# Optimization experiments

Hardware: AMD Instinct MI355X
Metric: run time of the kernel (lower is better)

## Reference

```python
import jax, jax.numpy as jnp
import numpy as np

B, P, N, E = 32, 1024, 1024, 128
HQ = 128  # head_num * qkv_dim == embedding_dim
SQRT_E = 11.313708498984761
LOGIT_CLIP = 10.0


def setup_inputs() -> dict:
    key = jax.random.key(0)
    ks = jax.random.split(key, 16)
    s = 1.0 / np.sqrt(E)
    return {
        "encoded_nodes": jax.random.normal(ks[0], (B, N, E), jnp.float32),
        "encoded_q1": jax.random.normal(ks[1], (B, P, E), jnp.float32),
        "encoded_q2": jax.random.normal(ks[2], (B, P, E), jnp.float32),
        "encoded_last_node": jax.random.normal(ks[3], (B, P, E), jnp.float32),
        "load": jax.random.uniform(ks[4], (B, P), jnp.float32),
        "left": jax.random.uniform(ks[5], (B, P), jnp.float32),
        "cur_dist": jax.random.uniform(ks[6], (B, P, N), jnp.float32),
        "log_scale": jnp.ones((), jnp.float32),
        "ninf_mask": jnp.zeros((B, P, N), jnp.float32),
        "Wq1": jax.random.normal(ks[7], (E, HQ), jnp.float32) * s,
        "Wq2": jax.random.normal(ks[8], (E, HQ), jnp.float32) * s,
        "Wq_last": jax.random.normal(ks[9], (E + 2, HQ), jnp.float32) * s,
        "Wk": jax.random.normal(ks[10], (E, HQ), jnp.float32) * s,
        "Wv": jax.random.normal(ks[11], (E, HQ), jnp.float32) * s,
        "AFT_dist_alpha": jnp.ones((1,), jnp.float32),
        "probs_dist_alpha": jnp.ones((1,), jnp.float32),
    }


def reference(encoded_nodes, encoded_q1, encoded_q2, encoded_last_node, load, left,
              cur_dist, log_scale, ninf_mask, Wq1, Wq2, Wq_last, Wk, Wv,
              AFT_dist_alpha, probs_dist_alpha):
    # set_kv / set_q1 / set_q2
    k = encoded_nodes @ Wk                      # [B,N,HQ]
    v = encoded_nodes @ Wv                      # [B,N,HQ]
    single_head_key = jnp.swapaxes(encoded_nodes, 1, 2)  # [B,E,N]
    q1 = encoded_q1 @ Wq1                       # [B,P,HQ]
    q2 = encoded_q2 @ Wq2

    input_cat = jnp.concatenate([encoded_last_node, load[:, :, None], left[:, :, None]], axis=2)
    q_last = input_cat @ Wq_last                # [B,P,HQ]
    q = q1 + q2 + q_last

    cur_dist_out = -cur_dist                    # [B,P,N]
    sigmoid_q = jax.nn.sigmoid(q)
    bias_scale = log_scale * AFT_dist_alpha[0] * cur_dist_out + ninf_mask
    e_bias = jnp.exp(bias_scale)                # [B,P,N]
    ek = jnp.exp(k)                             # [B,N,HQ]
    num = jnp.nan_to_num(jnp.einsum('bpn,bnd->bpd', e_bias, ek * v))
    den = jnp.nan_to_num(jnp.einsum('bpn,bnd->bpd', e_bias, ek)) + 1e-20
    AFT_out = sigmoid_q * (num / den)           # [B,P,HQ]

    score = jnp.einsum('bpd,bdn->bpn', AFT_out, single_head_key)
    score_scaled = score / SQRT_E + log_scale * probs_dist_alpha[0] * cur_dist_out
    score_clipped = LOGIT_CLIP * jnp.tanh(score_scaled)
    probs = jax.nn.softmax(score_clipped + ninf_mask, axis=2)
    return probs
```

## Files before the change

kernel.cpp:

```cpp
#include <hip/hip_runtime.h>
#include <math.h>

#define Bb 32
#define Pp 1024
#define Nn 1024

typedef unsigned short u16;
typedef __bf16 bf16x8 __attribute__((ext_vector_type(8)));
typedef float f32x4 __attribute__((ext_vector_type(4)));
typedef u16 us8 __attribute__((ext_vector_type(8)));
typedef u16 us4 __attribute__((ext_vector_type(4)));

#define MFMA __builtin_amdgcn_mfma_f32_16x16x32_bf16

static constexpr float INV_SQRT_E = 0.08838834764831845f;

__device__ __forceinline__ bf16x8 asbf(us8 v) { return __builtin_bit_cast(bf16x8, v); }

__device__ __forceinline__ void bsplit(float x, u16& h, u16& l) {
  unsigned u = __float_as_uint(x);
  unsigned r = u + 0x7FFF + ((u >> 16) & 1);
  h = (u16)(r >> 16);
  float hf = __uint_as_float((unsigned)h << 16);
  float lof = x - hf;
  unsigned u2 = __float_as_uint(lof);
  unsigned r2 = u2 + 0x7FFF + ((u2 >> 16) & 1);
  l = (u16)(r2 >> 16);
}

__device__ __forceinline__ void tsplit(float x, u16& h, u16& l) {
  unsigned u = __float_as_uint(x);
  h = (u16)(u >> 16);
  float lof = x - __uint_as_float(u & 0xFFFF0000u);
  l = (u16)(__float_as_uint(lof) >> 16);
}

__device__ __forceinline__ float fast_tanh(float x) {
  float ax = fabsf(x);
  float t = __expf(-2.0f * ax);
  float r = (1.0f - t) / (1.0f + t);
  return copysignf(r, x);
}

__global__ __launch_bounds__(256) void prep_weights(
    const float* __restrict__ Wq1, const float* __restrict__ Wq2,
    const float* __restrict__ Wql, const float* __restrict__ Wk,
    const float* __restrict__ Wv, u16* __restrict__ wcat_hi, u16* __restrict__ wcat_lo,
    u16* __restrict__ wkv_hi, u16* __restrict__ wkv_lo) {
  int t = threadIdx.x;
  if (blockIdx.x == 0) {
    for (int i = t; i < 128 * 384; i += 256) {
      int c = i / 384, k = i % 384;
      float v = (k < 128) ? Wq1[k * 128 + c]
                          : (k < 256) ? Wq2[(k - 128) * 128 + c] : Wql[(k - 256) * 128 + c];
      u16 h, l;
      bsplit(v, h, l);
      wcat_hi[i] = h;
      wcat_lo[i] = l;
    }
  } else {
    for (int i = t; i < 256 * 128; i += 256) {
      int c = i >> 7, k = i & 127;
      float v = (c < 128) ? Wk[k * 128 + c] : Wv[k * 128 + (c - 128)];
      u16 h, l;
      bsplit(v, h, l);
      wkv_hi[i] = h;
      wkv_lo[i] = l;
    }
  }
}

__global__ __launch_bounds__(256, 1) void kv_prep(
    const float* __restrict__ nodes, const u16* __restrict__ wkv_hi,
    const u16* __restrict__ wkv_lo, u16* __restrict__ ekkP_hi, u16* __restrict__ ekkP_lo,
    u16* __restrict__ nodesP_hi, u16* __restrict__ nodesP_lo) {
  __shared__ u16 a_hi[32 * 136], a_lo[32 * 136];
  __shared__ float kvbuf[32 * 264];
  const int t = threadIdx.x;
  const int xcd = blockIdx.x & 7, jj = blockIdx.x >> 3;
  const int b = xcd * 4 + (jj >> 5);
  const int n0 = (jj & 31) * 32;
  for (int i = t; i < 4096; i += 256) {
    int n = i >> 7, d = i & 127;
    float v = nodes[((long)(b * 1024 + n0 + n)) * 128 + d];
    u16 h, l;
    bsplit(v, h, l);
    a_hi[n * 136 + d] = h;
    a_lo[n * 136 + d] = l;
  }
  __syncthreads();
  const int lane = t & 63, w = t >> 6;
  const int lr = lane & 15, lg = lane >> 4;
  f32x4 acc0[2][4] = {}, acc1[2][4] = {};
#pragma unroll
  for (int ks = 0; ks < 4; ++ks) {
    us8 ah[2], al[2];
#pragma unroll
    for (int mt = 0; mt < 2; ++mt) {
      int ro = (lr + 16 * mt) * 136 + ks * 32 + lg * 8;
      ah[mt] = *(const us8*)&a_hi[ro];
      al[mt] = *(const us8*)&a_lo[ro];
    }
    us8 bh[4], bl[4];
#pragma unroll
    for (int cc = 0; cc < 4; ++cc) {
      long off = (long)((w * 4 + cc) * 16 + lr) * 128 + ks * 32 + lg * 8;
      bh[cc] = *(const us8*)&wkv_hi[off];
      bl[cc] = *(const us8*)&wkv_lo[off];
    }
#pragma unroll
    for (int mt = 0; mt < 2; ++mt)
#pragma unroll
      for (int cc = 0; cc < 4; ++cc) {
        acc0[mt][cc] = MFMA(asbf(ah[mt]), asbf(bh[cc]), acc0[mt][cc], 0, 0, 0);
        acc1[mt][cc] = MFMA(asbf(al[mt]), asbf(bh[cc]), acc1[mt][cc], 0, 0, 0);
        acc1[mt][cc] = MFMA(asbf(ah[mt]), asbf(bl[cc]), acc1[mt][cc], 0, 0, 0);
      }
  }
#pragma unroll
  for (int mt = 0; mt < 2; ++mt)
#pragma unroll
    for (int cc = 0; cc < 4; ++cc) {
      int c = (w * 4 + cc) * 16 + lr;
#pragma unroll
      for (int r = 0; r < 4; ++r)
        kvbuf[(lg * 4 + r + 16 * mt) * 264 + c] = acc0[mt][cc][r] + acc1[mt][cc][r];
    }
  __syncthreads();
#pragma unroll
  for (int jo = 0; jo < 4; ++jo) {
    int c = jo * 64 + (t & 63);
    int i4 = t >> 6;
    int kcol = (c < 128) ? c : (c - 128);
    us8 h8, l8;
#pragma unroll
    for (int jq = 0; jq < 8; ++jq) {
      int n = i4 * 8 + jq;
      float kv = kvbuf[n * 264 + kcol];
      float ek = __expf(kv);
      float val = (c < 128) ? ek * kvbuf[n * 264 + c + 128] : ek;
      u16 h, l;
      bsplit(val, h, l);
      h8[jq] = h;
      l8[jq] = l;
    }
    long o = (((long)b * 128 + (n0 >> 3) + i4) * 256 + c) * 8;
    *(us8*)&ekkP_hi[o] = h8;
    *(us8*)&ekkP_lo[o] = l8;
  }
  {
    int pl = t >> 7, r = t & 127;
    int dgrp = r >> 3, nb = r & 7;
    const u16* src = pl ? a_lo : a_hi;
    u16* dst = pl ? nodesP_lo : nodesP_hi;
#pragma unroll
    for (int i = 0; i < 4; ++i) {
      int n = nb + 8 * i;
      us8 v = *(const us8*)&src[n * 136 + dgrp * 8];
      *(us8*)&dst[(((long)(b * 16 + dgrp)) * 1024 + n0 + n) * 8] = v;
    }
  }
}

__global__ __launch_bounds__(256) void qsig_prep(
    const float* __restrict__ q1m, const float* __restrict__ q2m,
    const float* __restrict__ lnm, const float* __restrict__ loadv,
    const float* __restrict__ leftv, const float* __restrict__ Wql,
    const u16* __restrict__ wcat_hi, const u16* __restrict__ wcat_lo,
    float* __restrict__ qsig) {
  const int t = threadIdx.x;
  const int lane = t & 63, w = t >> 6;
  const int lr = lane & 15, lg = lane >> 4;
  const long p0 = (long)blockIdx.x * 16;
  const long arow = p0 + lr;
  f32x4 qacc[2] = {};
#pragma unroll 2
  for (int s = 0; s < 12; ++s) {
    const float* __restrict__ src = (s < 4) ? q1m : (s < 8) ? q2m : lnm;
    long ao = arow * 128 + (s & 3) * 32 + lg * 8;
    float4 a0 = *(const float4*)&src[ao];
    float4 a1 = *(const float4*)&src[ao + 4];
    float av[8] = {a0.x, a0.y, a0.z, a0.w, a1.x, a1.y, a1.z, a1.w};
    us8 ah, al;
#pragma unroll
    for (int jq = 0; jq < 8; ++jq) {
      u16 hh, ll;
      tsplit(av[jq], hh, ll);
      ah[jq] = hh;
      al[jq] = ll;
    }
#pragma unroll
    for (int cf = 0; cf < 2; ++cf) {
      int c = w * 32 + cf * 16 + lr;
      us8 bh = *(const us8*)&wcat_hi[c * 384 + s * 32 + lg * 8];
      us8 bl = *(const us8*)&wcat_lo[c * 384 + s * 32 + lg * 8];
      qacc[cf] = MFMA(asbf(ah), asbf(bh), qacc[cf], 0, 0, 0);
      qacc[cf] = MFMA(asbf(al), asbf(bh), qacc[cf], 0, 0, 0);
      qacc[cf] = MFMA(asbf(ah), asbf(bl), qacc[cf], 0, 0, 0);
    }
  }
#pragma unroll
  for (int cf = 0; cf < 2; ++cf) {
    int c = w * 32 + cf * 16 + lr;
    float wl1 = Wql[128 * 128 + c], wl2 = Wql[129 * 128 + c];
#pragma unroll
    for (int r = 0; r < 4; ++r) {
      int row = lg * 4 + r;
      float qv = qacc[cf][r] + loadv[p0 + row] * wl1 + leftv[p0 + row] * wl2;
      qsig[(p0 + row) * 128 + c] = 1.0f / (1.0f + __expf(-qv));
    }
  }
}

__global__ __launch_bounds__(256, 2) void ndaft_gemm(
    const float* __restrict__ cdist, const float* __restrict__ ninf,
    const u16* __restrict__ ekkP_hi, const u16* __restrict__ ekkP_lo,
    const float* __restrict__ qsig, u16* __restrict__ aftP_hi,
    u16* __restrict__ aftP_lo, u16* __restrict__ bias16,
    const float* __restrict__ logs, const float* __restrict__ aal,
    const float* __restrict__ pal) {
  __shared__ u16 lds[20480];
  const int t = threadIdx.x;
  const int lane = t & 63, w = t >> 6;
  const int lr = lane & 15, lg = lane >> 4;
  const int wr = w >> 1, wc = w & 1;
  const int xcd = blockIdx.x & 7, g = blockIdx.x >> 3;
  const int b = xcd * 4 + (g & 3);
  const int pt = g >> 2;
  const long bp = (long)b * Pp + pt * 64;
  const float c1 = logs[0] * aal[0];
  const float c2 = logs[0] * pal[0];

  const int srow = t >> 2, soct = t & 3;
  const long arow = bp + srow;
  const long tbase = (arow >> 4) * 32768;
  const int pr = srow & 15, ptile = srow >> 4;

  float4 d0, d1, f0, f1;
  us8 bst[8];
  auto load_regs = [&](int s) {
    long ao = arow * 1024 + s * 32 + soct * 8;
    d0 = *(const float4*)&cdist[ao];
    d1 = *(const float4*)&cdist[ao + 4];
    f0 = *(const float4*)&ninf[ao];
    f1 = *(const float4*)&ninf[ao + 4];
#pragma unroll
    for (int i = 0; i < 8; ++i) {
      int u = i * 256 + t;
      int oct = u >> 9, pl = (u >> 8) & 1, c = u & 255;
      const u16* bP = pl ? ekkP_lo : ekkP_hi;
      bst[i] = *(const us8*)&bP[(((long)b * 128 + s * 4 + oct) * 256 + c) * 8];
    }
  };

  us8 ebh, ebl;
  auto compute_eb = [&](int s) {
    float dv[8] = {d0.x, d0.y, d0.z, d0.w, d1.x, d1.y, d1.z, d1.w};
    float nv[8] = {f0.x, f0.y, f0.z, f0.w, f1.x, f1.y, f1.z, f1.w};
    us8 q8;
#pragma unroll
    for (int jq = 0; jq < 8; ++jq) {
      float e = __expf(fmaf(-c1, dv[jq], nv[jq]));
      u16 h, l;
      tsplit(e, h, l);
      ebh[jq] = h;
      ebl[jq] = l;
      float x = fminf(fmaxf(c2 * dv[jq], 0.f), 15.999f);
      q8[jq] = (nv[jq] < -1e5f) ? (u16)0xFFFF : (u16)(x * 4096.f + 0.5f);
    }
    *(us8*)&bias16[tbase + ((s * 4 + soct) * 16 + pr) * 8] = q8;
  };

  auto write_lds = [&]() {
    *(us8*)&lds[((ptile * 2 + 0) * 4 + soct) * 128 + pr * 8] = ebh;
    *(us8*)&lds[((ptile * 2 + 1) * 4 + soct) * 128 + pr * 8] = ebl;
#pragma unroll
    for (int i = 0; i < 8; ++i) {
      int u = i * 256 + t;
      int oct = u >> 9, pl = (u >> 8) & 1, c = u & 255;
      *(us8*)&lds[4096 + ((oct * 2 + pl) * 256 + c) * 8] = bst[i];
    }
  };

  f32x4 acc[2][8] = {};
  load_regs(0);
  for (int s = 0; s < 32; ++s) {
    compute_eb(s);
    __syncthreads();
    write_lds();
    __syncthreads();
    if (s < 31) load_regs(s + 1);
    us8 ah[2], al[2];
#pragma unroll
    for (int mt = 0; mt < 2; ++mt) {
      int ptl = wr * 2 + mt;
      ah[mt] = *(const us8*)&lds[((ptl * 2 + 0) * 4 + lg) * 128 + lr * 8];
      al[mt] = *(const us8*)&lds[((ptl * 2 + 1) * 4 + lg) * 128 + lr * 8];
    }
#pragma unroll
    for (int ct = 0; ct < 8; ++ct) {
      int c = (ct < 4) ? (wc * 64 + ct * 16 + lr) : (128 + wc * 64 + (ct - 4) * 16 + lr);
      us8 bh = *(const us8*)&lds[4096 + ((lg * 2 + 0) * 256 + c) * 8];
      us8 bl = *(const us8*)&lds[4096 + ((lg * 2 + 1) * 256 + c) * 8];
#pragma unroll
      for (int mt = 0; mt < 2; ++mt) {
        acc[mt][ct] = MFMA(asbf(ah[mt]), asbf(bh), acc[mt][ct], 0, 0, 0);
        acc[mt][ct] = MFMA(asbf(al[mt]), asbf(bh), acc[mt][ct], 0, 0, 0);
        acc[mt][ct] = MFMA(asbf(ah[mt]), asbf(bl), acc[mt][ct], 0, 0, 0);
      }
    }
  }
#pragma unroll
  for (int mt = 0; mt < 2; ++mt)
#pragma unroll
    for (int ct = 0; ct < 4; ++ct) {
      int cn = wc * 64 + ct * 16 + lr;
      int nc = cn >> 3, jq = cn & 7;
#pragma unroll
      for (int r = 0; r < 4; ++r) {
        long gr = bp + wr * 32 + mt * 16 + lg * 4 + r;
        float sig = qsig[gr * 128 + cn];
        float aftv = sig * (acc[mt][ct][r] / (acc[mt][ct + 4][r] + 1e-20f));
        u16 h, l;
        bsplit(aftv, h, l);
        long idx = (gr >> 4) * 2048 + (nc * 16 + (gr & 15)) * 8 + jq;
        aftP_hi[idx] = h;
        aftP_lo[idx] = l;
      }
    }
}

__global__ __launch_bounds__(512, 4) void score_softmax(
    const u16* bias16, const u16* __restrict__ aftP_hi, const u16* __restrict__ aftP_lo,
    const u16* __restrict__ nodesP_hi, const u16* __restrict__ nodesP_lo,
    float* out) {
  __shared__ float sbuf[32 * 264];
  __shared__ float psum[32 * 4];
  __shared__ float invb[32];
  const int t = threadIdx.x;
  const int lane = t & 63, w = t >> 6;
  const int lr = lane & 15, lg = lane >> 4;
  const int rg = w & 1, cg = w >> 1;
  const int xcd = blockIdx.x & 7, j = blockIdx.x >> 3;
  const int b = xcd * 4 + (j >> 5);
  const int p0 = (j & 31) * 32;
  const long bp = (long)b * Pp + p0;
  const int tileb = b * 64 + (p0 >> 4);

  f32x4 sacc[16] = {};
#pragma unroll
  for (int ks = 0; ks < 4; ++ks) {
    long aoff = (long)(tileb + rg) * 2048 + ((long)((ks * 4 + lg) * 16 + lr)) * 8;
    us8 ah = *(const us8*)&aftP_hi[aoff];
    us8 al = *(const us8*)&aftP_lo[aoff];
    long nb = ((long)(b * 16 + ks * 4 + lg)) * 1024;
#pragma unroll
    for (int cf = 0; cf < 16; ++cf) {
      long o = (nb + cg * 256 + cf * 16 + lr) * 8;
      us8 bh = *(const us8*)&nodesP_hi[o];
      us8 bl = *(const us8*)&nodesP_lo[o];
      sacc[cf] = MFMA(asbf(bh), asbf(ah), sacc[cf], 0, 0, 0);
      sacc[cf] = MFMA(asbf(bl), asbf(ah), sacc[cf], 0, 0, 0);
      sacc[cf] = MFMA(asbf(bh), asbf(al), sacc[cf], 0, 0, 0);
    }
  }

  const long btile = (long)(tileb + rg) * 32768;
  float rs = 0.f;
#pragma unroll
  for (int cf = 0; cf < 16; ++cf) {
    int nc = cg * 32 + cf * 2 + (lg >> 1);
    int j0 = (lg & 1) * 4;
    us4 q4 = *(const us4*)&bias16[btile + (nc * 16 + lr) * 8 + j0];
#pragma unroll
    for (int r = 0; r < 4; ++r) {
      u16 qv = q4[r];
      float sv = fmaf(sacc[cf][r], INV_SQRT_E, (float)qv * -2.44140625e-4f);
      float e = __expf(10.0f * fast_tanh(sv));
      e = (qv == (u16)0xFFFF) ? 0.f : e;
      sacc[cf][r] = e;
      rs += e;
    }
  }
  rs += __shfl_xor(rs, 16);
  rs += __shfl_xor(rs, 32);
  if (lg == 0) psum[(rg * 16 + lr) * 4 + cg] = rs;
  __syncthreads();
  if (t < 32)
    invb[t] = 1.0f / (psum[t * 4] + psum[t * 4 + 1] + psum[t * 4 + 2] + psum[t * 4 + 3]);
  __syncthreads();

  const float inv = invb[rg * 16 + lr];
#pragma unroll 1
  for (int c = 0; c < 4; ++c) {
    if (cg == c) {
      int prow = rg * 16 + lr;
#pragma unroll
      for (int cf = 0; cf < 16; ++cf) {
        float4 v;
        v.x = sacc[cf][0] * inv;
        v.y = sacc[cf][1] * inv;
        v.z = sacc[cf][2] * inv;
        v.w = sacc[cf][3] * inv;
        *(float4*)&sbuf[prow * 264 + cf * 16 + lg * 4] = v;
      }
    }
    __syncthreads();
    {
      int row = t >> 4, cq = t & 15;
      long ro = (bp + row) * (long)Nn + c * 256;
#pragma unroll
      for (int i = 0; i < 4; ++i)
        *(float4*)&out[ro + cq * 4 + i * 64] =
            *(const float4*)&sbuf[row * 264 + cq * 4 + i * 64];
    }
    __syncthreads();
  }
}

extern "C" void kernel_launch(void* const* d_in, const int* in_sizes, int n_in,
                              void* d_out, int out_size, void* d_ws, size_t ws_size,
                              hipStream_t stream) {
  const float* nodes = (const float*)d_in[0];
  const float* q1m = (const float*)d_in[1];
  const float* q2m = (const float*)d_in[2];
  const float* lnm = (const float*)d_in[3];
  const float* loadv = (const float*)d_in[4];
  const float* leftv = (const float*)d_in[5];
  const float* cdist = (const float*)d_in[6];
  const float* logs = (const float*)d_in[7];
  const float* ninf = (const float*)d_in[8];
  const float* Wq1 = (const float*)d_in[9];
  const float* Wq2 = (const float*)d_in[10];
  const float* Wql = (const float*)d_in[11];
  const float* Wk = (const float*)d_in[12];
  const float* Wv = (const float*)d_in[13];
  const float* aalpha = (const float*)d_in[14];
  const float* palpha = (const float*)d_in[15];

  char* ws = (char*)d_ws;
  u16* ekkP_hi = (u16*)ws;
  u16* ekkP_lo = (u16*)(ws + (16ul << 20));
  u16* nodesP_hi = (u16*)(ws + (32ul << 20));
  u16* nodesP_lo = (u16*)(ws + (40ul << 20));
  float* qsig = (float*)(ws + (48ul << 20));
  u16* aftP_hi = (u16*)(ws + (64ul << 20));
  u16* aftP_lo = (u16*)(ws + (72ul << 20));
  u16* wcat_hi = (u16*)(ws + (80ul << 20));
  u16* wcat_lo = wcat_hi + 128 * 384;
  u16* wkv_hi = wcat_lo + 128 * 384;
  u16* wkv_lo = wkv_hi + 256 * 128;
  u16* bias16 = (u16*)d_out;

  prep_weights<<<2, 256, 0, stream>>>(Wq1, Wq2, Wql, Wk, Wv, wcat_hi, wcat_lo, wkv_hi, wkv_lo);
  kv_prep<<<Bb * Nn / 32, 256, 0, stream>>>(nodes, wkv_hi, wkv_lo, ekkP_hi, ekkP_lo,
                                            nodesP_hi, nodesP_lo);
  qsig_prep<<<2048, 256, 0, stream>>>(q1m, q2m, lnm, loadv, leftv, Wql, wcat_hi, wcat_lo,
                                      qsig);
  ndaft_gemm<<<512, 256, 0, stream>>>(cdist, ninf, ekkP_hi, ekkP_lo, qsig, aftP_hi,
                                      aftP_lo, bias16, logs, aalpha, palpha);
  score_softmax<<<Bb * Pp / 32, 512, 0, stream>>>(
      bias16, aftP_hi, aftP_lo, nodesP_hi, nodesP_lo, (float*)d_out);
}
```

Before: 375.0 us.

## Halve row tiles in AFT GEMM and score kernels, drop LDS output staging

ndaft_gemm now handles 32 query rows per block instead of 64, with twice as many blocks, a launch-bounds occupancy hint of 3 and a smaller LDS buffer. Only half the threads compute the exp-bias tile. score_softmax moves to 16-row, 256-thread blocks that store normalized probabilities straight from registers instead of staging them through LDS, and it prefetches node B-fragments two steps ahead. The tanh/exp epilogue and the AFT division use a hardware reciprocal. The cost is that the ekk operand is re-read twice as often and output stores are less coalesced.

```diff
diff --git a/kernel.cpp b/kernel.cpp
--- a/kernel.cpp
+++ b/kernel.cpp
@@ -35,11 +35,13 @@
   l = (u16)(__float_as_uint(lof) >> 16);
 }
 
-__device__ __forceinline__ float fast_tanh(float x) {
-  float ax = fabsf(x);
-  float t = __expf(-2.0f * ax);
-  float r = (1.0f - t) / (1.0f + t);
-  return copysignf(r, x);
+__device__ __forceinline__ float exp10tanh(float s) {
+  float ax = fabsf(s);
+  float u = __expf(-2.0f * ax);
+  float r = __builtin_amdgcn_rcpf(1.0f + u);
+  float tt = fmaf(-2.0f * u, r, 1.0f);
+  tt = copysignf(tt, s);
+  return __expf(10.0f * tt);
 }
 
 __global__ __launch_bounds__(256) void prep_weights(
@@ -212,14 +214,14 @@
   }
 }
 
-__global__ __launch_bounds__(256, 2) void ndaft_gemm(
+__global__ __launch_bounds__(256, 3) void ndaft_gemm(
     const float* __restrict__ cdist, const float* __restrict__ ninf,
     const u16* __restrict__ ekkP_hi, const u16* __restrict__ ekkP_lo,
     const float* __restrict__ qsig, u16* __restrict__ aftP_hi,
     u16* __restrict__ aftP_lo, u16* __restrict__ bias16,
     const float* __restrict__ logs, const float* __restrict__ aal,
     const float* __restrict__ pal) {
-  __shared__ u16 lds[20480];
+  __shared__ u16 lds[18432];
   const int t = threadIdx.x;
   const int lane = t & 63, w = t >> 6;
   const int lr = lane & 15, lg = lane >> 4;
@@ -227,11 +229,12 @@
   const int xcd = blockIdx.x & 7, g = blockIdx.x >> 3;
   const int b = xcd * 4 + (g & 3);
   const int pt = g >> 2;
-  const long bp = (long)b * Pp + pt * 64;
+  const long bp = (long)b * Pp + pt * 32;
   const float c1 = logs[0] * aal[0];
   const float c2 = logs[0] * pal[0];
 
-  const int srow = t >> 2, soct = t & 3;
+  const int srow = (t < 128) ? (t >> 2) : 0;
+  const int soct = t & 3;
   const long arow = bp + srow;
   const long tbase = (arow >> 4) * 32768;
   const int pr = srow & 15, ptile = srow >> 4;
@@ -239,11 +242,13 @@
   float4 d0, d1, f0, f1;
   us8 bst[8];
   auto load_regs = [&](int s) {
-    long ao = arow * 1024 + s * 32 + soct * 8;
-    d0 = *(const float4*)&cdist[ao];
-    d1 = *(const float4*)&cdist[ao + 4];
-    f0 = *(const float4*)&ninf[ao];
-    f1 = *(const float4*)&ninf[ao + 4];
+    if (t < 128) {
+      long ao = arow * 1024 + s * 32 + soct * 8;
+      d0 = *(const float4*)&cdist[ao];
+      d1 = *(const float4*)&cdist[ao + 4];
+      f0 = *(const float4*)&ninf[ao];
+      f1 = *(const float4*)&ninf[ao + 4];
+    }
 #pragma unroll
     for (int i = 0; i < 8; ++i) {
       int u = i * 256 + t;
@@ -255,6 +260,7 @@
 
   us8 ebh, ebl;
   auto compute_eb = [&](int s) {
+    if (t >= 128) return;
     float dv[8] = {d0.x, d0.y, d0.z, d0.w, d1.x, d1.y, d1.z, d1.w};
     float nv[8] = {f0.x, f0.y, f0.z, f0.w, f1.x, f1.y, f1.z, f1.w};
     us8 q8;
@@ -272,17 +278,19 @@
   };
 
   auto write_lds = [&]() {
-    *(us8*)&lds[((ptile * 2 + 0) * 4 + soct) * 128 + pr * 8] = ebh;
-    *(us8*)&lds[((ptile * 2 + 1) * 4 + soct) * 128 + pr * 8] = ebl;
+    if (t < 128) {
+      *(us8*)&lds[((ptile * 2 + 0) * 4 + soct) * 128 + pr * 8] = ebh;
+      *(us8*)&lds[((ptile * 2 + 1) * 4 + soct) * 128 + pr * 8] = ebl;
+    }
 #pragma unroll
     for (int i = 0; i < 8; ++i) {
       int u = i * 256 + t;
       int oct = u >> 9, pl = (u >> 8) & 1, c = u & 255;
-      *(us8*)&lds[4096 + ((oct * 2 + pl) * 256 + c) * 8] = bst[i];
+      *(us8*)&lds[2048 + ((oct * 2 + pl) * 256 + c) * 8] = bst[i];
     }
   };
 
-  f32x4 acc[2][8] = {};
+  f32x4 acc[8] = {};
   load_regs(0);
   for (int s = 0; s < 32; ++s) {
     compute_eb(s);
@@ -290,93 +298,90 @@
     write_lds();
     __syncthreads();
     if (s < 31) load_regs(s + 1);
-    us8 ah[2], al[2];
-#pragma unroll
-    for (int mt = 0; mt < 2; ++mt) {
-      int ptl = wr * 2 + mt;
-      ah[mt] = *(const us8*)&lds[((ptl * 2 + 0) * 4 + lg) * 128 + lr * 8];
-      al[mt] = *(const us8*)&lds[((ptl * 2 + 1) * 4 + lg) * 128 + lr * 8];
-    }
+    us8 ah = *(const us8*)&lds[((wr * 2 + 0) * 4 + lg) * 128 + lr * 8];
+    us8 al = *(const us8*)&lds[((wr * 2 + 1) * 4 + lg) * 128 + lr * 8];
 #pragma unroll
     for (int ct = 0; ct < 8; ++ct) {
       int c = (ct < 4) ? (wc * 64 + ct * 16 + lr) : (128 + wc * 64 + (ct - 4) * 16 + lr);
-      us8 bh = *(const us8*)&lds[4096 + ((lg * 2 + 0) * 256 + c) * 8];
-      us8 bl = *(const us8*)&lds[4096 + ((lg * 2 + 1) * 256 + c) * 8];
-#pragma unroll
-      for (int mt = 0; mt < 2; ++mt) {
-        acc[mt][ct] = MFMA(asbf(ah[mt]), asbf(bh), acc[mt][ct], 0, 0, 0);
-        acc[mt][ct] = MFMA(asbf(al[mt]), asbf(bh), acc[mt][ct], 0, 0, 0);
-        acc[mt][ct] = MFMA(asbf(ah[mt]), asbf(bl), acc[mt][ct], 0, 0, 0);
-      }
-    }
-  }
-#pragma unroll
-  for (int mt = 0; mt < 2; ++mt)
-#pragma unroll
-    for (int ct = 0; ct < 4; ++ct) {
-      int cn = wc * 64 + ct * 16 + lr;
-      int nc = cn >> 3, jq = cn & 7;
-#pragma unroll
-      for (int r = 0; r < 4; ++r) {
-        long gr = bp + wr * 32 + mt * 16 + lg * 4 + r;
-        float sig = qsig[gr * 128 + cn];
-        float aftv = sig * (acc[mt][ct][r] / (acc[mt][ct + 4][r] + 1e-20f));
-        u16 h, l;
-        bsplit(aftv, h, l);
-        long idx = (gr >> 4) * 2048 + (nc * 16 + (gr & 15)) * 8 + jq;
-        aftP_hi[idx] = h;
-        aftP_lo[idx] = l;
-      }
-    }
-}
-
-__global__ __launch_bounds__(512, 4) void score_softmax(
+      us8 bh = *(const us8*)&lds[2048 + ((lg * 2 + 0) * 256 + c) * 8];
+      us8 bl = *(const us8*)&lds[2048 + ((lg * 2 + 1) * 256 + c) * 8];
+      acc[ct] = MFMA(asbf(ah), asbf(bh), acc[ct], 0, 0, 0);
+      acc[ct] = MFMA(asbf(al), asbf(bh), acc[ct], 0, 0, 0);
+      acc[ct] = MFMA(asbf(ah), asbf(bl), acc[ct], 0, 0, 0);
+    }
+  }
+#pragma unroll
+  for (int ct = 0; ct < 4; ++ct) {
+    int cn = wc * 64 + ct * 16 + lr;
+    int nc = cn >> 3, jq = cn & 7;
+#pragma unroll
+    for (int r = 0; r < 4; ++r) {
+      long gr = bp + wr * 16 + lg * 4 + r;
+      float sig = qsig[gr * 128 + cn];
+      float aftv = sig * acc[ct][r] * __builtin_amdgcn_rcpf(acc[ct + 4][r] + 1e-20f);
+      u16 h, l;
+      bsplit(aftv, h, l);
+      long idx = (gr >> 4) * 2048 + (nc * 16 + (gr & 15)) * 8 + jq;
+      aftP_hi[idx] = h;
+      aftP_lo[idx] = l;
+    }
+  }
+}
+
+__global__ __launch_bounds__(256, 4) void score_softmax(
     const u16* bias16, const u16* __restrict__ aftP_hi, const u16* __restrict__ aftP_lo,
     const u16* __restrict__ nodesP_hi, const u16* __restrict__ nodesP_lo,
     float* out) {
-  __shared__ float sbuf[32 * 264];
-  __shared__ float psum[32 * 4];
-  __shared__ float invb[32];
+  __shared__ float psum[16 * 4];
+  __shared__ float invb[16];
   const int t = threadIdx.x;
   const int lane = t & 63, w = t >> 6;
   const int lr = lane & 15, lg = lane >> 4;
-  const int rg = w & 1, cg = w >> 1;
   const int xcd = blockIdx.x & 7, j = blockIdx.x >> 3;
-  const int b = xcd * 4 + (j >> 5);
-  const int p0 = (j & 31) * 32;
+  const int b = xcd * 4 + (j >> 6);
+  const int tl = j & 63;
+  const int p0 = tl * 16;
   const long bp = (long)b * Pp + p0;
-  const int tileb = b * 64 + (p0 >> 4);
+  const int tile = b * 64 + tl;
 
   f32x4 sacc[16] = {};
 #pragma unroll
   for (int ks = 0; ks < 4; ++ks) {
-    long aoff = (long)(tileb + rg) * 2048 + ((long)((ks * 4 + lg) * 16 + lr)) * 8;
+    long aoff = (long)tile * 2048 + ((long)((ks * 4 + lg) * 16 + lr)) * 8;
     us8 ah = *(const us8*)&aftP_hi[aoff];
     us8 al = *(const us8*)&aftP_lo[aoff];
     long nb = ((long)(b * 16 + ks * 4 + lg)) * 1024;
+    auto bld = [&](int cf, us8& bh, us8& bl) {
+      long o = (nb + w * 256 + cf * 16 + lr) * 8;
+      bh = *(const us8*)&nodesP_hi[o];
+      bl = *(const us8*)&nodesP_lo[o];
+    };
+    us8 bh0, bl0, bh1, bl1;
+    bld(0, bh0, bl0);
+    bld(1, bh1, bl1);
 #pragma unroll
     for (int cf = 0; cf < 16; ++cf) {
-      long o = (nb + cg * 256 + cf * 16 + lr) * 8;
-      us8 bh = *(const us8*)&nodesP_hi[o];
-      us8 bl = *(const us8*)&nodesP_lo[o];
-      sacc[cf] = MFMA(asbf(bh), asbf(ah), sacc[cf], 0, 0, 0);
-      sacc[cf] = MFMA(asbf(bl), asbf(ah), sacc[cf], 0, 0, 0);
-      sacc[cf] = MFMA(asbf(bh), asbf(al), sacc[cf], 0, 0, 0);
-    }
-  }
-
-  const long btile = (long)(tileb + rg) * 32768;
+      us8 nh = bh1, nl = bl1;
+      if (cf < 14) bld(cf + 2, nh, nl);
+      sacc[cf] = MFMA(asbf(bh0), asbf(ah), sacc[cf], 0, 0, 0);
+      sacc[cf] = MFMA(asbf(bl0), asbf(ah), sacc[cf], 0, 0, 0);
+      sacc[cf] = MFMA(asbf(bh0), asbf(al), sacc[cf], 0, 0, 0);
+      bh0 = bh1; bl0 = bl1; bh1 = nh; bl1 = nl;
+    }
+  }
+
+  const long btile = (long)tile * 32768;
   float rs = 0.f;
 #pragma unroll
   for (int cf = 0; cf < 16; ++cf) {
-    int nc = cg * 32 + cf * 2 + (lg >> 1);
+    int nc = w * 32 + cf * 2 + (lg >> 1);
     int j0 = (lg & 1) * 4;
     us4 q4 = *(const us4*)&bias16[btile + (nc * 16 + lr) * 8 + j0];
 #pragma unroll
     for (int r = 0; r < 4; ++r) {
       u16 qv = q4[r];
       float sv = fmaf(sacc[cf][r], INV_SQRT_E, (float)qv * -2.44140625e-4f);
-      float e = __expf(10.0f * fast_tanh(sv));
+      float e = exp10tanh(sv);
       e = (qv == (u16)0xFFFF) ? 0.f : e;
       sacc[cf][r] = e;
       rs += e;
@@ -384,37 +389,22 @@
   }
   rs += __shfl_xor(rs, 16);
   rs += __shfl_xor(rs, 32);
-  if (lg == 0) psum[(rg * 16 + lr) * 4 + cg] = rs;
+  if (lane < 16) psum[lr * 4 + w] = rs;
   __syncthreads();
-  if (t < 32)
+  if (t < 16)
     invb[t] = 1.0f / (psum[t * 4] + psum[t * 4 + 1] + psum[t * 4 + 2] + psum[t * 4 + 3]);
   __syncthreads();
 
-  const float inv = invb[rg * 16 + lr];
-#pragma unroll 1
-  for (int c = 0; c < 4; ++c) {
-    if (cg == c) {
-      int prow = rg * 16 + lr;
-#pragma unroll
-      for (int cf = 0; cf < 16; ++cf) {
-        float4 v;
-        v.x = sacc[cf][0] * inv;
-        v.y = sacc[cf][1] * inv;
-        v.z = sacc[cf][2] * inv;
-        v.w = sacc[cf][3] * inv;
-        *(float4*)&sbuf[prow * 264 + cf * 16 + lg * 4] = v;
-      }
-    }
-    __syncthreads();
-    {
-      int row = t >> 4, cq = t & 15;
-      long ro = (bp + row) * (long)Nn + c * 256;
-#pragma unroll
-      for (int i = 0; i < 4; ++i)
-        *(float4*)&out[ro + cq * 4 + i * 64] =
-            *(const float4*)&sbuf[row * 264 + cq * 4 + i * 64];
-    }
-    __syncthreads();
+  const float inv = invb[lr];
+  const long ro = (bp + lr) * (long)Nn + w * 256;
+#pragma unroll
+  for (int cf = 0; cf < 16; ++cf) {
+    float4 v;
+    v.x = sacc[cf][0] * inv;
+    v.y = sacc[cf][1] * inv;
+    v.z = sacc[cf][2] * inv;
+    v.w = sacc[cf][3] * inv;
+    *(float4*)&out[ro + cf * 16 + lg * 4] = v;
   }
 }
 
@@ -457,8 +447,8 @@
                                             nodesP_hi, nodesP_lo);
   qsig_prep<<<2048, 256, 0, stream>>>(q1m, q2m, lnm, loadv, leftv, Wql, wcat_hi, wcat_lo,
                                       qsig);
-  ndaft_gemm<<<512, 256, 0, stream>>>(cdist, ninf, ekkP_hi, ekkP_lo, qsig, aftP_hi,
-                                      aftP_lo, bias16, logs, aalpha, palpha);
-  score_softmax<<<Bb * Pp / 32, 512, 0, stream>>>(
+  ndaft_gemm<<<1024, 256, 0, stream>>>(cdist, ninf, ekkP_hi, ekkP_lo, qsig, aftP_hi,
+                                       aftP_lo, bias16, logs, aalpha, palpha);
+  score_softmax<<<Bb * Pp / 16, 256, 0, stream>>>(
       bias16, aftP_hi, aftP_lo, nodesP_hi, nodesP_lo, (float*)d_out);
 }
```

Result: no change. 373.0 us (-0.5%).
